# Kernel tuning notes

Hardware: AMD Instinct MI355X
Metric: run time of the kernel (lower is better)

Reference implementation:

```python
import jax, jax.numpy as jnp
import numpy as np

# Effective integer sampling displacement per kernel tap = (kernel offset from
# center) + (fixed learned-free offset baked into the torch forward).
# torch tap order is row-major over the 3x3 kernel; offsets listed in source:
# tap0:(-1,-1)+(0,-2)=(-1,-3)  tap1:(-1,0)+(0,-1)=(-1,-1)  tap2:(-1,1)+(0,0)=(-1,1)
# tap3:(0,-1)+(0,1)=(0,0)      tap4:(0,0)+(0,2)=(0,2)      tap5:(0,1)+(-2,0)=(-2,1)
# tap6:(1,-1)+(-1,0)=(0,-1)    tap7:(1,0)+(1,0)=(2,0)      tap8:(1,1)+(2,0)=(3,1)
TAPS = [(-1, -3), (-1, -1), (-1, 1), (0, 0), (0, 2), (-2, 1), (0, -1), (2, 0), (3, 1)]
PAD = 3  # max |displacement|
DOWN_SCALE = 4  # heatmap_size // pooler_resolution


def deform_conv_fixed(x, w):
    """Deformable conv with fixed integer offsets == sum of shifted GEMMs.
    Integer offsets make bilinear sampling an exact gather; out-of-bounds -> 0
    (matches deform conv zero-padding semantics).
    x: [N,C,H,W], w: [O,C,3,3] -> [N,O,H,W]
    """
    N, C, H, W = x.shape
    xp = jnp.pad(x, ((0, 0), (0, 0), (PAD, PAD), (PAD, PAD)))
    wf = w.reshape(w.shape[0], C, 9)  # [O,C,9], taps row-major
    y = jnp.zeros((N, w.shape[0], H, W), dtype=x.dtype)
    for t, (dh, dw) in enumerate(TAPS):
        xs = xp[:, :, PAD + dh:PAD + dh + H, PAD + dw:PAD + dw + W]
        y = y + jnp.einsum('nchw,oc->nohw', xs, wf[:, :, t])
    return y


def max_pool(x, k):
    N, C, H, W = x.shape
    return x.reshape(N, C, H // k, k, W // k, k).max(axis=(3, 5))


def setup_inputs() -> dict:
    key = jax.random.key(0)
    ks = jax.random.split(key, 6)
    N, C_IN, R = 128, 512, 28
    P1 = 25  # NUM_PATCHES + 1
    HID, HM = 256, 112
    s_in = 0.02
    return {
        'features': jax.random.normal(ks[0], (N, C_IN, R, R), jnp.float32),
        'fine_segm': jax.random.normal(ks[1], (N, P1, HM, HM), jnp.float32),
        'w1': jax.random.normal(ks[2], (HID, C_IN + P1, 3, 3), jnp.float32) * s_in,
        'w2': jax.random.normal(ks[3], (HID, HID, 3, 3), jnp.float32) * s_in,
        'w3': jax.random.normal(ks[4], (HID, HID, 3, 3), jnp.float32) * s_in,
        'w4': jax.random.normal(ks[5], (HID, HID, 3, 3), jnp.float32) * s_in,
    }


def reference(features, fine_segm, w1, w2, w3, w4):
    pooled = max_pool(fine_segm, DOWN_SCALE)  # [N,25,28,28]
    x = jnp.concatenate([features, jax.lax.stop_gradient(pooled)], axis=1)
    for w in (w1, w2, w3, w4):
        x = jax.nn.relu(deform_conv_fixed(x, w))
    return x
```

## Files before the change

kernel.cpp:

```cpp
#include <hip/hip_runtime.h>
#include <stdint.h>

typedef short bf16x8 __attribute__((ext_vector_type(8)));
typedef float f32x4 __attribute__((ext_vector_type(4)));

#define N_IMG 128
#define C_IN 512
#define NP1 25
#define C1 537
#define C1P 576
#define HID 256
#define RR 28
#define PLANE 784
#define P_TOTAL (N_IMG * PLANE)

#define TILE_H 4
#define HALO_H 9
#define HALO_W 33
#define RC_SLOTS (HALO_H * HALO_W)
#define GRAN_PAD 2560
#define BUF_U16 (GRAN_PAD * 8)

__device__ __align__(16) uint16_t g_zeropage[2048];

__device__ __forceinline__ uint16_t f2bf(float f) {
  union { float f; uint32_t u; } v; v.f = f;
  return (uint16_t)((v.u + 0x7fffu + ((v.u >> 16) & 1u)) >> 16);
}

__device__ __forceinline__ void load16(void* lds, const void* g) {
  __builtin_amdgcn_global_load_lds(
      (__attribute__((address_space(1))) void*)(g),
      (__attribute__((address_space(3))) void*)(lds), 16, 0, 0);
}

__global__ void pool_kernel(const float* __restrict__ fs, float* __restrict__ pooled) {
  int u = blockIdx.x * 256 + threadIdx.x;
  if (u >= N_IMG * NP1 * PLANE) return;
  int w = u % RR;
  int tmp = u / RR;
  int h = tmp % RR; tmp /= RR;
  int c = tmp % NP1;
  int n = tmp / NP1;
  const float* base = fs + (((size_t)(n * NP1 + c)) * 112 + h * 4) * 112 + w * 4;
  float m = -INFINITY;
#pragma unroll
  for (int i = 0; i < 4; i++) {
    float4 v = *(const float4*)(base + (size_t)i * 112);
    m = fmaxf(m, fmaxf(fmaxf(v.x, v.y), fmaxf(v.z, v.w)));
  }
  pooled[u] = m;
}

__global__ void build_x0(const float* __restrict__ feat, const float* __restrict__ pooled,
                         uint16_t* __restrict__ X0) {
  __shared__ float tile[64][65];
  const int n = blockIdx.z;
  const int c0 = blockIdx.y * 64;
  const int p0 = blockIdx.x * 64;
  const int tx = threadIdx.x & 63;
  const int ty = threadIdx.x >> 6;
  const int p = p0 + tx;
#pragma unroll
  for (int k = 0; k < 16; k++) {
    const int cl = ty + k * 4;
    const int c = c0 + cl;
    float v = 0.f;
    if (p < PLANE) {
      if (c < C_IN)
        v = feat[((size_t)(n * C_IN + c)) * PLANE + p];
      else if (c < C1)
        v = pooled[((size_t)(n * NP1 + (c - C_IN))) * PLANE + p];
    }
    tile[cl][tx] = v;
  }
  __syncthreads();
#pragma unroll
  for (int k = 0; k < 2; k++) {
    const int u = threadIdx.x + k * 256;
    const int pl = u >> 3;
    const int ch = u & 7;
    if (p0 + pl < PLANE) {
      bf16x8 v;
#pragma unroll
      for (int e = 0; e < 8; e++) v[e] = (short)f2bf(tile[ch * 8 + e][pl]);
      *(bf16x8*)&X0[((size_t)n * PLANE + p0 + pl) * C1P + c0 + ch * 8] = v;
    }
  }
}

__global__ void wconv_kernel(const float* __restrict__ w, uint16_t* __restrict__ wbf,
                             int C, int CPAD) {
  const int NK = CPAD / 64;
  int v = blockIdx.x * 256 + threadIdx.x;
  if (v >= 9 * HID * CPAD) return;
  const int e = v & 7;
  const int lane = (v >> 3) & 63;
  const int j = (v >> 9) & 3;
  const int kh = (v >> 11) & 1;
  const int wv = (v >> 12) & 3;
  const int u = v >> 14;
  const int kc = u % NK;
  const int t = u / NK;
  const int o = wv * 64 + j * 16 + (lane & 15);
  const int ch = kc * 64 + kh * 32 + (lane >> 4) * 8 + e;
  uint16_t out = 0;
  if (ch < C) out = f2bf(w[((size_t)(o * C + ch)) * 9 + t]);
  wbf[v] = out;
}

template <int CPAD, bool FINAL>
__global__ __launch_bounds__(256, 2) void conv_halo(const uint16_t* __restrict__ Xin,
                                                    const uint16_t* __restrict__ Wt,
                                                    uint16_t* __restrict__ Yout,
                                                    float* __restrict__ Fout) {
  constexpr int NK = CPAD / 64;
  constexpr int TDH[9] = {-1, -1, -1, 0, 0, -2, 0, 2, 3};
  constexpr int TDW[9] = {-3, -1, 1, 0, 2, 1, -1, 0, 1};

  __shared__ __align__(16) uint16_t Abuf[2][BUF_U16];

  const int tid = threadIdx.x;
  const int lane = tid & 63;
  const int wv = tid >> 6;
  const int l15 = lane & 15;
  const int q = lane >> 4;
  const int ocw = wv * 64;

  const int bid = blockIdx.x;
  const int logical = (bid & 7) * 112 + (bid >> 3);
  const int n = logical / 7;
  const int band = logical - n * 7;
  const int h0 = band * TILE_H;

  const char* srcp[10];
#pragma unroll
  for (int it = 0; it < 10; ++it) {
    const int s = it * 256 + tid;
    const int rc = s >> 3;
    const int r = rc / HALO_W;
    const int c = rc - r * HALO_W;
    const int g = (s & 7) ^ ((c + 4 * r) & 7);
    const int ih = h0 - 2 + r;
    const int ic = c - 3;
    const bool valid = (rc < RC_SLOTS) & (ih >= 0) & (ih < RR) & (ic >= 0) & (ic < RR);
    srcp[it] = valid
        ? (const char*)(Xin + ((size_t)(n * PLANE + ih * RR + ic)) * CPAD + g * 8)
        : (const char*)g_zeropage;
  }

  int baseoff[7], key0[7];
#pragma unroll
  for (int m = 0; m < 7; ++m) {
    const int pos = m * 16 + l15;
    const int hr = pos / RR;
    const int wc = pos - hr * RR;
    baseoff[m] = ((hr + 2) * HALO_W + (wc + 3)) * 128;
    key0[m] = ((wc + 3) + 4 * (hr + 2)) & 7;
  }

  const bf16x8* __restrict__ Wf = (const bf16x8*)Wt;
  const int wfbase = wv * 512 + lane;

  f32x4 acc[7][4];
#pragma unroll
  for (int m = 0; m < 7; ++m)
#pragma unroll
    for (int j = 0; j < 4; ++j) acc[m][j] = (f32x4){0.f, 0.f, 0.f, 0.f};

#pragma unroll
  for (int it = 0; it < 10; ++it)
    load16((char*)Abuf[0] + it * 4096 + wv * 1024, srcp[it]);

#pragma unroll 1
  for (int kc = 0; kc < NK; ++kc) {
    const uint16_t* curbuf = Abuf[kc & 1];
    if (kc + 1 < NK) {
      char* nb = (char*)Abuf[(kc + 1) & 1];
      const int off = (kc + 1) * 128;
#pragma unroll
      for (int it = 0; it < 10; ++it)
        load16(nb + it * 4096 + wv * 1024, srcp[it] + off);
      asm volatile("s_waitcnt vmcnt(10)" ::: "memory");
    } else {
      asm volatile("s_waitcnt vmcnt(0)" ::: "memory");
    }
    __builtin_amdgcn_s_barrier();
    asm volatile("" ::: "memory");

    const bf16x8* __restrict__ Wkc = Wf + (size_t)kc * 2048 + wfbase;
#pragma unroll
    for (int t = 0; t < 9; ++t) {
      const int dh = TDH[t], dw = TDW[t];
      bf16x8 bfrag[2][4];
#pragma unroll
      for (int kh = 0; kh < 2; ++kh)
#pragma unroll
        for (int j = 0; j < 4; ++j)
          bfrag[kh][j] = Wkc[(size_t)t * (NK * 2048) + kh * 256 + j * 64];
      const int toff = (dh * HALO_W + dw) * 128;
#pragma unroll
      for (int kh = 0; kh < 2; ++kh) {
        const int kq = kh * 4 + q;
        bf16x8 af[7];
#pragma unroll
        for (int m = 0; m < 7; ++m) {
          const int keyt = (key0[m] + dw + 4 * dh) & 7;
          const int boff = baseoff[m] + toff + ((kq ^ keyt) << 4);
          af[m] = *(const bf16x8*)((const char*)curbuf + boff);
        }
        __builtin_amdgcn_s_setprio(1);
#pragma unroll
        for (int m = 0; m < 7; ++m)
#pragma unroll
          for (int j = 0; j < 4; ++j)
            acc[m][j] = __builtin_amdgcn_mfma_f32_16x16x32_bf16(af[m], bfrag[kh][j],
                                                                acc[m][j], 0, 0, 0);
        __builtin_amdgcn_s_setprio(0);
      }
    }
    asm volatile("" ::: "memory");
    __builtin_amdgcn_s_barrier();
  }

  const int pbase = n * PLANE + h0 * RR;
  if (!FINAL) {
#pragma unroll
    for (int m = 0; m < 7; ++m) {
#pragma unroll
      for (int r = 0; r < 4; ++r) {
        const int gpos = pbase + m * 16 + q * 4 + r;
        uint16_t* row = Yout + (size_t)gpos * HID + ocw + l15;
#pragma unroll
        for (int j = 0; j < 4; ++j) row[j * 16] = f2bf(fmaxf(acc[m][j][r], 0.f));
      }
    }
  } else {
#pragma unroll
    for (int m = 0; m < 7; ++m) {
      const int p4 = m * 16 + q * 4;
      const int hh = p4 / RR;
      const int ww = p4 - hh * RR;
#pragma unroll
      for (int j = 0; j < 4; ++j) {
        const int o = ocw + j * 16 + l15;
        f32x4 v = acc[m][j];
        v[0] = fmaxf(v[0], 0.f);
        v[1] = fmaxf(v[1], 0.f);
        v[2] = fmaxf(v[2], 0.f);
        v[3] = fmaxf(v[3], 0.f);
        *(f32x4*)(Fout + ((size_t)(n * HID + o)) * PLANE + (h0 + hh) * RR + ww) = v;
      }
    }
  }
}

extern "C" void kernel_launch(void* const* d_in, const int* in_sizes, int n_in,
                              void* d_out, int out_size, void* d_ws, size_t ws_size,
                              hipStream_t stream) {
  const float* feat = (const float*)d_in[0];
  const float* fseg = (const float*)d_in[1];
  const float* w1 = (const float*)d_in[2];
  const float* w2 = (const float*)d_in[3];
  const float* w3 = (const float*)d_in[4];
  const float* w4 = (const float*)d_in[5];
  float* out = (float*)d_out;

  uint8_t* p = (uint8_t*)d_ws;
  uint16_t* X0 = (uint16_t*)p; p += (size_t)P_TOTAL * C1P * 2;
  uint16_t* XA = (uint16_t*)p; p += (size_t)P_TOTAL * HID * 2;
  uint16_t* XB = (uint16_t*)p; p += (size_t)P_TOTAL * HID * 2;
  float* pooled = (float*)p;   p += (size_t)N_IMG * NP1 * PLANE * 4;
  uint16_t* W1b = (uint16_t*)p; p += (size_t)9 * HID * C1P * 2;
  uint16_t* W2b = (uint16_t*)p; p += (size_t)9 * HID * HID * 2;
  uint16_t* W3b = (uint16_t*)p; p += (size_t)9 * HID * HID * 2;
  uint16_t* W4b = (uint16_t*)p; p += (size_t)9 * HID * HID * 2;

  pool_kernel<<<(N_IMG * NP1 * PLANE + 255) / 256, 256, 0, stream>>>(fseg, pooled);
  wconv_kernel<<<(9 * HID * C1P + 255) / 256, 256, 0, stream>>>(w1, W1b, C1, C1P);
  wconv_kernel<<<(9 * HID * HID + 255) / 256, 256, 0, stream>>>(w2, W2b, HID, HID);
  wconv_kernel<<<(9 * HID * HID + 255) / 256, 256, 0, stream>>>(w3, W3b, HID, HID);
  wconv_kernel<<<(9 * HID * HID + 255) / 256, 256, 0, stream>>>(w4, W4b, HID, HID);
  build_x0<<<dim3(13, 9, N_IMG), 256, 0, stream>>>(feat, pooled, X0);

  const int cgrid = P_TOTAL / (TILE_H * RR);
  conv_halo<C1P, false><<<cgrid, 256, 0, stream>>>(X0, W1b, XA, nullptr);
  conv_halo<HID, false><<<cgrid, 256, 0, stream>>>(XA, W2b, XB, nullptr);
  conv_halo<HID, false><<<cgrid, 256, 0, stream>>>(XB, W3b, XA, nullptr);
  conv_halo<HID, true><<<cgrid, 256, 0, stream>>>(XA, W4b, nullptr, out);
}
```

Baseline: 998.5 us.

## Split output channels across 8 waves per block to raise occupancy

Each conv block now runs 512 threads (8 waves), with each wave computing 32 output channels instead of 64. This halves the per-wave accumulator and weight-fragment registers, and launch bounds are raised so 4 blocks of 512 threads can share a CU. The halo-load loop is spread across more threads, and the per-row base offset and swizzle key are packed into a single register. The aim is more resident waves to hide LDS and global latency, at the cost of each A fragment from LDS being reused across half as many MFMAs, which doubles LDS read traffic per MFMA.

Measured after the change: 1.628 ms. +63.1%, slower.

```diff
diff --git a/kernel.cpp b/kernel.cpp
--- a/kernel.cpp
+++ b/kernel.cpp
@@ -110,7 +110,7 @@
 }
 
 template <int CPAD, bool FINAL>
-__global__ __launch_bounds__(256, 2) void conv_halo(const uint16_t* __restrict__ Xin,
+__global__ __launch_bounds__(512, 4) void conv_halo(const uint16_t* __restrict__ Xin,
                                                     const uint16_t* __restrict__ Wt,
                                                     uint16_t* __restrict__ Yout,
                                                     float* __restrict__ Fout) {
@@ -125,7 +125,9 @@
   const int wv = tid >> 6;
   const int l15 = lane & 15;
   const int q = lane >> 4;
-  const int ocw = wv * 64;
+  const int ocw = wv * 32;
+  const int wvq = wv >> 1;
+  const int jb = (wv & 1) * 2;
 
   const int bid = blockIdx.x;
   const int logical = (bid & 7) * 112 + (bid >> 3);
@@ -133,10 +135,10 @@
   const int band = logical - n * 7;
   const int h0 = band * TILE_H;
 
-  const char* srcp[10];
-#pragma unroll
-  for (int it = 0; it < 10; ++it) {
-    const int s = it * 256 + tid;
+  const char* srcp[5];
+#pragma unroll
+  for (int it = 0; it < 5; ++it) {
+    const int s = it * 512 + tid;
     const int rc = s >> 3;
     const int r = rc / HALO_W;
     const int c = rc - r * HALO_W;
@@ -149,28 +151,26 @@
         : (const char*)g_zeropage;
   }
 
-  int baseoff[7], key0[7];
+  int kadr[7];
 #pragma unroll
   for (int m = 0; m < 7; ++m) {
     const int pos = m * 16 + l15;
     const int hr = pos / RR;
     const int wc = pos - hr * RR;
-    baseoff[m] = ((hr + 2) * HALO_W + (wc + 3)) * 128;
-    key0[m] = ((wc + 3) + 4 * (hr + 2)) & 7;
+    kadr[m] = (((hr + 2) * HALO_W + (wc + 3)) * 128) | (((wc + 3) + 4 * (hr + 2)) & 7);
   }
 
   const bf16x8* __restrict__ Wf = (const bf16x8*)Wt;
-  const int wfbase = wv * 512 + lane;
-
-  f32x4 acc[7][4];
+
+  f32x4 acc[7][2];
 #pragma unroll
   for (int m = 0; m < 7; ++m)
 #pragma unroll
-    for (int j = 0; j < 4; ++j) acc[m][j] = (f32x4){0.f, 0.f, 0.f, 0.f};
-
-#pragma unroll
-  for (int it = 0; it < 10; ++it)
-    load16((char*)Abuf[0] + it * 4096 + wv * 1024, srcp[it]);
+    for (int j = 0; j < 2; ++j) acc[m][j] = (f32x4){0.f, 0.f, 0.f, 0.f};
+
+#pragma unroll
+  for (int it = 0; it < 5; ++it)
+    load16((char*)Abuf[0] + it * 8192 + wv * 1024, srcp[it]);
 
 #pragma unroll 1
   for (int kc = 0; kc < NK; ++kc) {
@@ -179,43 +179,44 @@
       char* nb = (char*)Abuf[(kc + 1) & 1];
       const int off = (kc + 1) * 128;
 #pragma unroll
-      for (int it = 0; it < 10; ++it)
-        load16(nb + it * 4096 + wv * 1024, srcp[it] + off);
-      asm volatile("s_waitcnt vmcnt(10)" ::: "memory");
+      for (int it = 0; it < 5; ++it)
+        load16(nb + it * 8192 + wv * 1024, srcp[it] + off);
+      asm volatile("s_waitcnt vmcnt(5)" ::: "memory");
     } else {
       asm volatile("s_waitcnt vmcnt(0)" ::: "memory");
     }
     __builtin_amdgcn_s_barrier();
     asm volatile("" ::: "memory");
 
-    const bf16x8* __restrict__ Wkc = Wf + (size_t)kc * 2048 + wfbase;
 #pragma unroll
     for (int t = 0; t < 9; ++t) {
       const int dh = TDH[t], dw = TDW[t];
-      bf16x8 bfrag[2][4];
+      const size_t fbase = ((((size_t)t * NK + kc) * 4 + wvq) * 2) * 4 * 64 + lane;
+      bf16x8 bfrag[2][2];
 #pragma unroll
       for (int kh = 0; kh < 2; ++kh)
 #pragma unroll
-        for (int j = 0; j < 4; ++j)
-          bfrag[kh][j] = Wkc[(size_t)t * (NK * 2048) + kh * 256 + j * 64];
+        for (int jj = 0; jj < 2; ++jj)
+          bfrag[kh][jj] = Wf[fbase + (size_t)kh * 256 + (jb + jj) * 64];
       const int toff = (dh * HALO_W + dw) * 128;
+      const int dkey = dw + 4 * dh;
 #pragma unroll
       for (int kh = 0; kh < 2; ++kh) {
         const int kq = kh * 4 + q;
         bf16x8 af[7];
 #pragma unroll
         for (int m = 0; m < 7; ++m) {
-          const int keyt = (key0[m] + dw + 4 * dh) & 7;
-          const int boff = baseoff[m] + toff + ((kq ^ keyt) << 4);
+          const int keyt = ((kadr[m] & 7) + dkey) & 7;
+          const int boff = (kadr[m] & -128) + toff + ((kq ^ keyt) << 4);
           af[m] = *(const bf16x8*)((const char*)curbuf + boff);
         }
         __builtin_amdgcn_s_setprio(1);
 #pragma unroll
         for (int m = 0; m < 7; ++m)
 #pragma unroll
-          for (int j = 0; j < 4; ++j)
-            acc[m][j] = __builtin_amdgcn_mfma_f32_16x16x32_bf16(af[m], bfrag[kh][j],
-                                                                acc[m][j], 0, 0, 0);
+          for (int jj = 0; jj < 2; ++jj)
+            acc[m][jj] = __builtin_amdgcn_mfma_f32_16x16x32_bf16(af[m], bfrag[kh][jj],
+                                                                 acc[m][jj], 0, 0, 0);
         __builtin_amdgcn_s_setprio(0);
       }
     }
@@ -232,7 +233,7 @@
         const int gpos = pbase + m * 16 + q * 4 + r;
         uint16_t* row = Yout + (size_t)gpos * HID + ocw + l15;
 #pragma unroll
-        for (int j = 0; j < 4; ++j) row[j * 16] = f2bf(fmaxf(acc[m][j][r], 0.f));
+        for (int jj = 0; jj < 2; ++jj) row[jj * 16] = f2bf(fmaxf(acc[m][jj][r], 0.f));
       }
     }
   } else {
@@ -242,9 +243,9 @@
       const int hh = p4 / RR;
       const int ww = p4 - hh * RR;
 #pragma unroll
-      for (int j = 0; j < 4; ++j) {
-        const int o = ocw + j * 16 + l15;
-        f32x4 v = acc[m][j];
+      for (int jj = 0; jj < 2; ++jj) {
+        const int o = ocw + jj * 16 + l15;
+        f32x4 v = acc[m][jj];
         v[0] = fmaxf(v[0], 0.f);
         v[1] = fmaxf(v[1], 0.f);
         v[2] = fmaxf(v[2], 0.f);
@@ -284,8 +285,8 @@
   build_x0<<<dim3(13, 9, N_IMG), 256, 0, stream>>>(feat, pooled, X0);
 
   const int cgrid = P_TOTAL / (TILE_H * RR);
-  conv_halo<C1P, false><<<cgrid, 256, 0, stream>>>(X0, W1b, XA, nullptr);
-  conv_halo<HID, false><<<cgrid, 256, 0, stream>>>(XA, W2b, XB, nullptr);
-  conv_halo<HID, false><<<cgrid, 256, 0, stream>>>(XB, W3b, XA, nullptr);
-  conv_halo<HID, true><<<cgrid, 256, 0, stream>>>(XA, W4b, nullptr, out);
-}
+  conv_halo<C1P, false><<<cgrid, 512, 0, stream>>>(X0, W1b, XA, nullptr);
+  conv_halo<HID, false><<<cgrid, 512, 0, stream>>>(XA, W2b, XB, nullptr);
+  conv_halo<HID, false><<<cgrid, 512, 0, stream>>>(XB, W3b, XA, nullptr);
+  conv_halo<HID, true><<<cgrid, 512, 0, stream>>>(XA, W4b, nullptr, out);
+}
```
